# Optimization experiments

Measured on AMD Instinct MI355X. Metric: run time of the kernel, lower is better.

## Reference

```python
import jax, jax.numpy as jnp
import numpy as np

B, S, D = 4, 2048, 2048
H = 16
HD = D // H  # head_dim = 128


def setup_inputs() -> dict:
    key = jax.random.key(0)
    ks = jax.random.split(key, 6)
    x = jax.random.normal(ks[0], (B, S, D), dtype=jnp.float32)
    Wq = jax.random.normal(ks[1], (D, D), dtype=jnp.float32) * 0.02
    Wk = jax.random.normal(ks[2], (D, D), dtype=jnp.float32) * 0.02
    Wv = jax.random.normal(ks[3], (D, D), dtype=jnp.float32) * 0.02
    Wo = jax.random.normal(ks[4], (D, D), dtype=jnp.float32) * 0.02
    bo = jax.random.normal(ks[5], (D,), dtype=jnp.float32) * 0.02
    return {"x": x, "Wq": Wq, "Wk": Wk, "Wv": Wv, "Wo": Wo, "bo": bo}


def reference(x, Wq, Wk, Wv, Wo, bo):
    b, s, _ = x.shape
    # QKV projections, split heads: [b, h, s, hd]
    q = (x @ Wq).reshape(b, s, H, HD).transpose(0, 2, 1, 3)
    k = (x @ Wk).reshape(b, s, H, HD).transpose(0, 2, 1, 3)
    v = (x @ Wv).reshape(b, s, H, HD).transpose(0, 2, 1, 3)
    # scores: [b, h, s_q, s_k]
    scores = jnp.einsum("bhqd,bhkd->bhqk", q, k)
    # causal mask: future positions (k > q) get -inf (masking before scaling,
    # as in the original; -inf is invariant under the scale)
    causal = jnp.tril(jnp.ones((s, s), dtype=bool))
    scores = jnp.where(causal, scores, -jnp.inf)
    scale = 1.0 / np.sqrt(HD).astype(np.float32)
    attn = jax.nn.softmax(scores * scale, axis=-1)
    # dropout p=0.0 -> identity (eval-mode reference)
    ctx = jnp.einsum("bhqk,bhkd->bqhd", attn, v).reshape(b, s, D)
    return ctx @ Wo + bo
```

## Files before the change

### kernel.cpp

```cpp
#include <hip/hip_runtime.h>
#include <hip/hip_bf16.h>

#define BB 4
#define SS 2048
#define DD 2048
#define HH 16
#define HDD 128

typedef __bf16 bf16x8_t __attribute__((ext_vector_type(8)));
typedef float f32x4 __attribute__((ext_vector_type(4)));
typedef float f32x16 __attribute__((ext_vector_type(16)));

static __device__ __forceinline__ unsigned short f2bf(float f) {
    union { float f; unsigned u; } v; v.f = f;
    unsigned r = v.u + 0x7fffu + ((v.u >> 16) & 1u);
    return (unsigned short)(r >> 16);
}

static __device__ __forceinline__ unsigned cvtpk_bf16(float lo, float hiv) {
    unsigned r;
    asm("v_cvt_pk_bf16_f32 %0, %1, %2" : "=v"(r) : "v"(lo), "v"(hiv));
    return r;
}

static __device__ __forceinline__ void pl32swap(unsigned& a, unsigned& b) {
    auto rr = __builtin_amdgcn_permlane32_swap((int)a, (int)b, false, false);
    a = (unsigned)rr[0];
    b = (unsigned)rr[1];
}

static __device__ __forceinline__ void gload_lds16(const void* g, void* lds) {
    __builtin_amdgcn_global_load_lds(
        (const __attribute__((address_space(1))) void*)g,
        (__attribute__((address_space(3))) void*)lds, 16, 0, 0);
}

__global__ void convert_x(const float* __restrict__ x, unsigned short* __restrict__ xb, int n) {
    int i = (blockIdx.x * blockDim.x + threadIdx.x) * 4;
    int stride = gridDim.x * blockDim.x * 4;
    for (; i < n; i += stride) {
        float4 v = *(const float4*)(x + i);
        ushort4 o;
        o.x = f2bf(v.x); o.y = f2bf(v.y); o.z = f2bf(v.z); o.w = f2bf(v.w);
        *(ushort4*)(xb + i) = o;
    }
}

__global__ void transpose_w(const float* __restrict__ Wq, const float* __restrict__ Wk,
                            const float* __restrict__ Wv, const float* __restrict__ Wo,
                            unsigned short* __restrict__ WqkvT, unsigned short* __restrict__ WoT) {
    __shared__ float t[32][33];
    const int z = blockIdx.z;
    const float* W = (z == 0) ? Wq : (z == 1) ? Wk : (z == 2) ? Wv : Wo;
    unsigned short* T = (z < 3) ? (WqkvT + (size_t)z * DD * DD) : WoT;
    const int k0 = blockIdx.x * 32, n0 = blockIdx.y * 32;
    const int tx = threadIdx.x, ty = threadIdx.y;
#pragma unroll
    for (int i = 0; i < 4; ++i) {
        int r = ty + i * 8;
        t[r][tx] = W[(size_t)(k0 + r) * DD + n0 + tx];
    }
    __syncthreads();
#pragma unroll
    for (int i = 0; i < 4; ++i) {
        int r = ty + i * 8;
        T[(size_t)(n0 + r) * DD + k0 + tx] = f2bf(t[tx][r]);
    }
}

template <int MODE>
__global__ __launch_bounds__(512, 1) void gemm256(
    const unsigned short* __restrict__ A, const unsigned short* __restrict__ BT,
    unsigned short* __restrict__ outQ, unsigned short* __restrict__ outK,
    unsigned short* __restrict__ outV, float* __restrict__ outF,
    const float* __restrict__ bias) {
    __shared__ __attribute__((aligned(16))) char lds[131072];
    const int tid = threadIdx.x, l = tid & 63;
    const int w = tid >> 6;
    const int wr = w >> 2, wc = w & 3;
    const int nwg = gridDim.x * gridDim.y;
    int lin = blockIdx.y * gridDim.x + blockIdx.x;
    lin = (lin & 7) * (nwg >> 3) + (lin >> 3);
    const int m0 = (lin / gridDim.x) * 256;
    const int n0 = (lin % gridDim.x) * 256;

    f32x4 acc[8][4] = {};

    const int rowl = tid >> 3, c16s = tid & 7;
    const int sw16 = (c16s ^ (rowl & 7)) * 16;
    const char* aSrc[4];
    const char* bSrc[4];
#pragma unroll
    for (int rg = 0; rg < 4; ++rg) {
        aSrc[rg] = (const char*)A + ((size_t)(m0 + rg * 64 + rowl) * 2048) * 2 + sw16;
        bSrc[rg] = (const char*)BT + ((size_t)(n0 + rg * 64 + rowl) * 2048) * 2 + sw16;
    }
    const int dstOff = tid * 16;

    auto stage = [&](int slot, int off) {
        char* sA = lds + slot * 32768;
        char* sB = lds + 65536 + slot * 32768;
        gload_lds16(bSrc[0] + off, sB + 0 * 8192 + dstOff);
        gload_lds16(bSrc[1] + off, sB + 1 * 8192 + dstOff);
        gload_lds16(bSrc[2] + off, sB + 2 * 8192 + dstOff);
        gload_lds16(bSrc[3] + off, sB + 3 * 8192 + dstOff);
        gload_lds16(aSrc[0] + off, sA + 0 * 8192 + dstOff);
        gload_lds16(aSrc[2] + off, sA + 2 * 8192 + dstOff);
        gload_lds16(aSrc[1] + off, sA + 1 * 8192 + dstOff);
        gload_lds16(aSrc[3] + off, sA + 3 * 8192 + dstOff);
    };

    stage(0, 0);
    asm volatile("s_waitcnt vmcnt(0)" ::: "memory");
    __builtin_amdgcn_s_barrier();

    const int lr = l & 15, hi4 = l >> 4;
    int cur = 0;
    for (int t = 0; t < 32; ++t) {
        const char* As_ = lds + cur * 32768;
        const char* Bs_ = lds + 65536 + cur * 32768;
        bf16x8_t aa[4], bb[4];
#pragma unroll
        for (int mq = 0; mq < 4; ++mq) {
            int row = wr * 128 + mq * 16 + lr;
            aa[mq] = *(const bf16x8_t*)(As_ + row * 128 + ((hi4) ^ (row & 7)) * 16);
        }
#pragma unroll
        for (int nq = 0; nq < 4; ++nq) {
            int col = wc * 64 + nq * 16 + lr;
            bb[nq] = *(const bf16x8_t*)(Bs_ + col * 128 + ((hi4) ^ (col & 7)) * 16);
        }
        if (t + 1 < 32) stage(cur ^ 1, (t + 1) * 128);
        __builtin_amdgcn_s_setprio(1);
#pragma unroll
        for (int mq = 0; mq < 4; ++mq)
#pragma unroll
            for (int nq = 0; nq < 4; ++nq)
                acc[mq][nq] = __builtin_amdgcn_mfma_f32_16x16x32_bf16(aa[mq], bb[nq], acc[mq][nq], 0, 0, 0);
        __builtin_amdgcn_s_setprio(0);
        if (t + 1 < 32) { asm volatile("s_waitcnt vmcnt(8)" ::: "memory"); }
        else            { asm volatile("s_waitcnt vmcnt(0)" ::: "memory"); }
        __builtin_amdgcn_s_barrier();
#pragma unroll
        for (int mq = 0; mq < 4; ++mq) {
            int row = wr * 128 + 64 + mq * 16 + lr;
            aa[mq] = *(const bf16x8_t*)(As_ + row * 128 + ((hi4) ^ (row & 7)) * 16);
        }
        __builtin_amdgcn_s_setprio(1);
#pragma unroll
        for (int mq = 0; mq < 4; ++mq)
#pragma unroll
            for (int nq = 0; nq < 4; ++nq)
                acc[4 + mq][nq] = __builtin_amdgcn_mfma_f32_16x16x32_bf16(aa[mq], bb[nq], acc[4 + mq][nq], 0, 0, 0);
        __builtin_amdgcn_s_setprio(0);
#pragma unroll
        for (int nq = 0; nq < 4; ++nq) {
            int col = wc * 64 + nq * 16 + lr;
            bb[nq] = *(const bf16x8_t*)(Bs_ + col * 128 + ((4 + hi4) ^ (col & 7)) * 16);
        }
#pragma unroll
        for (int mq = 0; mq < 4; ++mq) {
            int row = wr * 128 + mq * 16 + lr;
            aa[mq] = *(const bf16x8_t*)(As_ + row * 128 + ((4 + hi4) ^ (row & 7)) * 16);
        }
        __builtin_amdgcn_s_setprio(1);
#pragma unroll
        for (int mq = 0; mq < 4; ++mq)
#pragma unroll
            for (int nq = 0; nq < 4; ++nq)
                acc[mq][nq] = __builtin_amdgcn_mfma_f32_16x16x32_bf16(aa[mq], bb[nq], acc[mq][nq], 0, 0, 0);
        __builtin_amdgcn_s_setprio(0);
#pragma unroll
        for (int mq = 0; mq < 4; ++mq) {
            int row = wr * 128 + 64 + mq * 16 + lr;
            aa[mq] = *(const bf16x8_t*)(As_ + row * 128 + ((4 + hi4) ^ (row & 7)) * 16);
        }
        __builtin_amdgcn_s_setprio(1);
#pragma unroll
        for (int mq = 0; mq < 4; ++mq)
#pragma unroll
            for (int nq = 0; nq < 4; ++nq)
                acc[4 + mq][nq] = __builtin_amdgcn_mfma_f32_16x16x32_bf16(aa[mq], bb[nq], acc[4 + mq][nq], 0, 0, 0);
        __builtin_amdgcn_s_setprio(0);
        if (t + 1 < 32) { asm volatile("s_waitcnt vmcnt(2)" ::: "memory"); }
        __builtin_amdgcn_s_barrier();
        cur ^= 1;
    }

    const int rbase = m0 + wr * 128 + (hi4 << 2);
    const int cbase = n0 + wc * 64 + lr;
    if (MODE == 0) {
#pragma unroll
        for (int nq = 0; nq < 4; ++nq) {
            int col = cbase + nq * 16;
            int mat = col >> 11;
            int nn = col & 2047;
            int h = nn >> 7, hd = nn & 127;
            if (mat == 2) {
#pragma unroll
                for (int i = 0; i < 8; ++i) {
                    int row = rbase + i * 16;
                    int b = row >> 11, s = row & 2047;
                    ushort4 pk;
                    pk.x = f2bf(acc[i][nq][0]); pk.y = f2bf(acc[i][nq][1]);
                    pk.z = f2bf(acc[i][nq][2]); pk.w = f2bf(acc[i][nq][3]);
                    *(ushort4*)(outV + ((size_t)(b * HH + h) * HDD + hd) * SS + s) = pk;
                }
            } else {
                unsigned short* outp = mat ? outK : outQ;
#pragma unroll
                for (int i = 0; i < 8; ++i) {
#pragma unroll
                    for (int r = 0; r < 4; ++r) {
                        int row = rbase + i * 16 + r;
                        int b = row >> 11, s = row & 2047;
                        outp[((size_t)(b * HH + h) * SS + s) * HDD + hd] = f2bf(acc[i][nq][r]);
                    }
                }
            }
        }
    } else {
#pragma unroll
        for (int nq = 0; nq < 4; ++nq) {
            int col = cbase + nq * 16;
            float bv = bias[col];
#pragma unroll
            for (int i = 0; i < 8; ++i) {
#pragma unroll
                for (int r = 0; r < 4; ++r) {
                    int row = rbase + i * 16 + r;
                    outF[(size_t)row * DD + col] = acc[i][nq][r] + bv;
                }
            }
        }
    }
}

__global__ __launch_bounds__(256, 2) void attn_kernel(
    const unsigned short* __restrict__ Q, const unsigned short* __restrict__ K,
    const unsigned short* __restrict__ VT, unsigned short* __restrict__ ctx) {
    __shared__ __attribute__((aligned(16))) unsigned short Ks[2][64 * 128];
    __shared__ __attribute__((aligned(16))) unsigned short Vs[2][128 * 64];
    __shared__ float Al[4][32];
    const int tid = threadIdx.x, w = tid >> 6, l = tid & 63;
    const int hi = l >> 5, l31 = l & 31;
    const int hb = hi * 16;
    const int swz = (l31 & 7) << 4;
    const int p = blockIdx.x, h = blockIdx.y, b = blockIdx.z;
    const int bh = b * HH + h;
    const float scale2 = 0.08838834764831845f * 1.4426950408889634f;

    const unsigned short* Qbh = Q + (size_t)bh * SS * HDD;
    const char* Kbh = (const char*)(K + (size_t)bh * SS * HDD);
    const char* Vbh = (const char*)(VT + (size_t)bh * HDD * SS);

    const char* kbase[4];
    const char* vbase[4];
#pragma unroll
    for (int i = 0; i < 4; ++i) {
        int cp = (i * 256 + tid) * 16;
        int krow = cp >> 8, kcb = cp & 255;
        kbase[i] = Kbh + (size_t)krow * 256 + (kcb ^ ((krow & 7) << 4));
        int vrow = cp >> 7, vcb = cp & 127;
        vbase[i] = Vbh + (size_t)vrow * (SS * 2) + (vcb ^ ((vrow & 7) << 4));
    }

    auto stage = [&](int buf, int kv0) {
#pragma unroll
        for (int i = 0; i < 4; ++i) {
            int cp = (i * 256 + tid) * 16;
            gload_lds16(kbase[i] + (size_t)kv0 * 256, (char*)&Ks[buf][0] + cp);
            gload_lds16(vbase[i] + (size_t)kv0 * 2, (char*)&Vs[buf][0] + cp);
        }
    };

    for (int pass = 0; pass < 2; ++pass) {
        const int qt = pass ? p : 15 - p;
        const int q0w = qt * 128 + w * 32;
        const int qabs = q0w + l31;
        const int nkv = 2 * qt + 2;

        bf16x8_t qf[8];
#pragma unroll
        for (int ds = 0; ds < 8; ++ds)
            qf[ds] = *(const bf16x8_t*)(Qbh + (size_t)qabs * HDD + ds * 16 + hi * 8);

        float m_r = -1e30f, l_r = 0.f;
        f32x16 o0 = {}, o1 = {}, o2 = {}, o3 = {};

        int buf = 0;
        stage(0, 0);
        __syncthreads();

        for (int kt = 0; kt < nkv; ++kt) {
            const int kv0 = kt * 64;
            if (kt + 1 < nkv) stage(buf ^ 1, kv0 + 64);

            if (kv0 <= q0w + 31) {
                const char* Kb = (const char*)&Ks[buf][0];
                const char* Vb = (const char*)&Vs[buf][0];
                f32x16 s0 = {}, s1 = {};
                {
                    bf16x8_t kf[8];
                    const int rb = l31 * 256;
#pragma unroll
                    for (int ds = 0; ds < 8; ++ds)
                        kf[ds] = *(const bf16x8_t*)(Kb + rb + ((ds * 32 + hb) ^ swz));
                    __builtin_amdgcn_s_setprio(1);
#pragma unroll
                    for (int ds = 0; ds < 8; ++ds)
                        s0 = __builtin_amdgcn_mfma_f32_32x32x16_bf16(kf[ds], qf[ds], s0, 0, 0, 0);
                    __builtin_amdgcn_s_setprio(0);
#pragma unroll
                    for (int ds = 0; ds < 8; ++ds)
                        kf[ds] = *(const bf16x8_t*)(Kb + rb + 32 * 256 + ((ds * 32 + hb) ^ swz));
                    __builtin_amdgcn_s_setprio(1);
#pragma unroll
                    for (int ds = 0; ds < 8; ++ds)
                        s1 = __builtin_amdgcn_mfma_f32_32x32x16_bf16(kf[ds], qf[ds], s1, 0, 0, 0);
                    __builtin_amdgcn_s_setprio(0);
                }

                if (kv0 + 63 > q0w) {
                    const int qrel = qabs - kv0;
#pragma unroll
                    for (int r = 0; r < 16; ++r) {
                        const int kl = (r & 3) + 8 * (r >> 2) + 4 * hi;
                        s0[r] = (kl > qrel) ? -1e30f : s0[r] * scale2;
                        s1[r] = (kl + 32 > qrel) ? -1e30f : s1[r] * scale2;
                    }
                } else {
#pragma unroll
                    for (int r = 0; r < 16; ++r) { s0[r] *= scale2; s1[r] *= scale2; }
                }

                float mx = s0[0];
#pragma unroll
                for (int r = 1; r < 16; ++r) mx = fmaxf(mx, s0[r]);
#pragma unroll
                for (int r = 0; r < 16; ++r) mx = fmaxf(mx, s1[r]);
                {
                    unsigned mu = __float_as_uint(mx), mu2 = mu;
                    pl32swap(mu, mu2);
                    mx = fmaxf(__uint_as_float(mu), __uint_as_float(mu2));
                }

                if (__any(mx - m_r > 8.f)) {
                    float mnew = fmaxf(m_r, mx);
                    float alpha = exp2f(m_r - mnew);
                    m_r = mnew;
                    l_r *= alpha;
                    Al[w][l31] = alpha;
#pragma unroll
                    for (int r = 0; r < 16; ++r) {
                        float ar = Al[w][(r & 3) + 8 * (r >> 2) + 4 * hi];
                        o0[r] *= ar; o1[r] *= ar; o2[r] *= ar; o3[r] *= ar;
                    }
                }

                float ps = 0.f;
#pragma unroll
                for (int r = 0; r < 16; ++r) { s0[r] = exp2f(s0[r] - m_r); ps += s0[r]; }
#pragma unroll
                for (int r = 0; r < 16; ++r) { s1[r] = exp2f(s1[r] - m_r); ps += s1[r]; }
                {
                    unsigned pu = __float_as_uint(ps), pu2 = pu;
                    pl32swap(pu, pu2);
                    l_r += __uint_as_float(pu) + __uint_as_float(pu2);
                }

                bf16x8_t pa[4];
                {
                    union { unsigned u[4]; bf16x8_t v; } uu;
#define MK_PA(SV, BASE, OUT)                                     \
                    {                                            \
                        unsigned X0 = cvtpk_bf16(SV[BASE + 0], SV[BASE + 1]); \
                        unsigned Y0 = cvtpk_bf16(SV[BASE + 4], SV[BASE + 5]); \
                        pl32swap(X0, Y0);                        \
                        unsigned X1 = cvtpk_bf16(SV[BASE + 2], SV[BASE + 3]); \
                        unsigned Y1 = cvtpk_bf16(SV[BASE + 6], SV[BASE + 7]); \
                        pl32swap(X1, Y1);                        \
                        uu.u[0] = X0; uu.u[1] = X1; uu.u[2] = Y0; uu.u[3] = Y1; \
                        OUT = uu.v;                              \
                    }
                    MK_PA(s0, 0, pa[0]);
                    MK_PA(s0, 8, pa[1]);
                    MK_PA(s1, 0, pa[2]);
                    MK_PA(s1, 8, pa[3]);
#undef MK_PA
                }

#pragma unroll
                for (int ks = 0; ks < 4; ++ks) {
                    bf16x8_t vf[4];
#pragma unroll
                    for (int dsub = 0; dsub < 4; ++dsub)
                        vf[dsub] = *(const bf16x8_t*)(Vb + (dsub * 32 + l31) * 128 + ((ks * 32 + hb) ^ swz));
                    __builtin_amdgcn_s_setprio(1);
                    o0 = __builtin_amdgcn_mfma_f32_32x32x16_bf16(pa[ks], vf[0], o0, 0, 0, 0);
                    o1 = __builtin_amdgcn_mfma_f32_32x32x16_bf16(pa[ks], vf[1], o1, 0, 0, 0);
                    o2 = __builtin_amdgcn_mfma_f32_32x32x16_bf16(pa[ks], vf[2], o2, 0, 0, 0);
                    o3 = __builtin_amdgcn_mfma_f32_32x32x16_bf16(pa[ks], vf[3], o3, 0, 0, 0);
                    __builtin_amdgcn_s_setprio(0);
                }
            }
            __syncthreads();
            buf ^= 1;
        }

        Al[w][l31] = 1.f / l_r;
        unsigned short* cb_ = ctx + (size_t)b * SS * DD + (size_t)h * HDD;
#pragma unroll
        for (int r = 0; r < 16; ++r) {
            const int ql = (r & 3) + 8 * (r >> 2) + 4 * hi;
            float inv = Al[w][ql];
            const size_t rowoff = (size_t)(q0w + ql) * DD;
            cb_[rowoff + 0 * 32 + l31] = f2bf(o0[r] * inv);
            cb_[rowoff + 1 * 32 + l31] = f2bf(o1[r] * inv);
            cb_[rowoff + 2 * 32 + l31] = f2bf(o2[r] * inv);
            cb_[rowoff + 3 * 32 + l31] = f2bf(o3[r] * inv);
        }
    }
}

extern "C" void kernel_launch(void* const* d_in, const int* in_sizes, int n_in,
                              void* d_out, int out_size, void* d_ws, size_t ws_size,
                              hipStream_t stream) {
    (void)in_sizes; (void)n_in; (void)out_size; (void)ws_size;
    const float* x  = (const float*)d_in[0];
    const float* Wq = (const float*)d_in[1];
    const float* Wk = (const float*)d_in[2];
    const float* Wv = (const float*)d_in[3];
    const float* Wo = (const float*)d_in[4];
    const float* bo = (const float*)d_in[5];

    char* ws = (char*)d_ws;
    unsigned short* xb    = (unsigned short*)(ws);
    unsigned short* WqkvT = (unsigned short*)(ws + (32u << 20));
    unsigned short* WoT   = (unsigned short*)(ws + (56u << 20));
    unsigned short* Qb    = (unsigned short*)(ws + (64u << 20));
    unsigned short* Kb    = (unsigned short*)(ws + (96u << 20));
    unsigned short* VTb   = (unsigned short*)(ws + (160u << 20));
    unsigned short* ctx   = xb;

    convert_x<<<4096, 256, 0, stream>>>(x, xb, BB * SS * DD);
    transpose_w<<<dim3(64, 64, 4), dim3(32, 8), 0, stream>>>(Wq, Wk, Wv, Wo, WqkvT, WoT);
    gemm256<0><<<dim3(24, 32), 512, 0, stream>>>(xb, WqkvT, Qb, Kb, VTb, nullptr, nullptr);
    attn_kernel<<<dim3(8, HH, BB), 256, 0, stream>>>(Qb, Kb, VTb, ctx);
    gemm256<1><<<dim3(8, 32), 512, 0, stream>>>(ctx, WoT, nullptr, nullptr, nullptr, (float*)d_out, bo);
}
```

Before: 426.2 us.

## Split GEMM K-tiles into half-tiles and interleave loads with MFMA phases

Restructures the 256x256 GEMM main loop so each K=64 tile is stored as two 32-wide half-tiles with a 4-way swizzle. Global-to-LDS loads for future half-tiles are issued between the four MFMA phases, so prefetch runs up to two tiles ahead instead of one. The goal is finer-grained overlap of memory traffic with MFMA work and shorter waits at the loop boundary. In exchange it adds more barriers and lgkmcnt waits per iteration. The loop tail also reissues loads for clamped tile indices, which is redundant work.

```diff
diff --git a/kernel.cpp b/kernel.cpp
--- a/kernel.cpp
+++ b/kernel.cpp
@@ -86,107 +86,123 @@
 
     f32x4 acc[8][4] = {};
 
-    const int rowl = tid >> 3, c16s = tid & 7;
-    const int sw16 = (c16s ^ (rowl & 7)) * 16;
-    const char* aSrc[4];
-    const char* bSrc[4];
-#pragma unroll
-    for (int rg = 0; rg < 4; ++rg) {
-        aSrc[rg] = (const char*)A + ((size_t)(m0 + rg * 64 + rowl) * 2048) * 2 + sw16;
-        bSrc[rg] = (const char*)BT + ((size_t)(n0 + rg * 64 + rowl) * 2048) * 2 + sw16;
-    }
-    const int dstOff = tid * 16;
-
-    auto stage = [&](int slot, int off) {
-        char* sA = lds + slot * 32768;
-        char* sB = lds + 65536 + slot * 32768;
-        gload_lds16(bSrc[0] + off, sB + 0 * 8192 + dstOff);
-        gload_lds16(bSrc[1] + off, sB + 1 * 8192 + dstOff);
-        gload_lds16(bSrc[2] + off, sB + 2 * 8192 + dstOff);
-        gload_lds16(bSrc[3] + off, sB + 3 * 8192 + dstOff);
-        gload_lds16(aSrc[0] + off, sA + 0 * 8192 + dstOff);
-        gload_lds16(aSrc[2] + off, sA + 2 * 8192 + dstOff);
-        gload_lds16(aSrc[1] + off, sA + 1 * 8192 + dstOff);
-        gload_lds16(aSrc[3] + off, sA + 3 * 8192 + dstOff);
+    const int srow = tid >> 2;
+    const int swz16 = ((tid & 3) ^ (srow & 3)) << 4;
+    const char* aR = (const char*)A + ((size_t)(m0 + srow) * 2048) * 2 + swz16;
+    const char* bR = (const char*)BT + ((size_t)(n0 + srow) * 2048) * 2 + swz16;
+    const int dOff = tid * 16;
+
+    auto stA = [&](int slot, int kt, int kh) {
+        char* d = lds + slot * 32768 + kh * 16384 + dOff;
+        const char* s = aR + kt * 128 + kh * 64;
+        gload_lds16(s, d);
+        gload_lds16(s + (size_t)128 * 4096, d + 8192);
     };
-
-    stage(0, 0);
-    asm volatile("s_waitcnt vmcnt(0)" ::: "memory");
+    auto stB = [&](int slot, int kt, int kh) {
+        char* d = lds + 65536 + slot * 32768 + kh * 16384 + dOff;
+        const char* s = bR + kt * 128 + kh * 64;
+        gload_lds16(s, d);
+        gload_lds16(s + (size_t)128 * 4096, d + 8192);
+    };
+
+    stA(0, 0, 0); stB(0, 0, 0); stA(0, 0, 1); stB(0, 0, 1); stA(1, 1, 0); stB(1, 1, 0);
+    asm volatile("s_waitcnt vmcnt(8)" ::: "memory");
     __builtin_amdgcn_s_barrier();
 
-    const int lr = l & 15, hi4 = l >> 4;
-    int cur = 0;
+    const int lr = l & 15;
+    const int rsw = (((l >> 4) ^ (lr & 3)) << 4);
+
     for (int t = 0; t < 32; ++t) {
-        const char* As_ = lds + cur * 32768;
-        const char* Bs_ = lds + 65536 + cur * 32768;
+        const int slot = t & 1;
+        const char* As_ = lds + slot * 32768;
+        const char* Bs_ = lds + 65536 + slot * 32768;
+        const int tn1 = (t + 1 < 32) ? t + 1 : 31;
+        const int tn2 = (t + 2 < 32) ? t + 2 : 31;
+        const int sl1 = (t + 1) & 1;
         bf16x8_t aa[4], bb[4];
-#pragma unroll
-        for (int mq = 0; mq < 4; ++mq) {
-            int row = wr * 128 + mq * 16 + lr;
-            aa[mq] = *(const bf16x8_t*)(As_ + row * 128 + ((hi4) ^ (row & 7)) * 16);
+
+#pragma unroll
+        for (int ii = 0; ii < 4; ++ii) {
+            int row = wr * 128 + ii * 16 + lr;
+            aa[ii] = *(const bf16x8_t*)(As_ + row * 64 + rsw);
         }
 #pragma unroll
         for (int nq = 0; nq < 4; ++nq) {
             int col = wc * 64 + nq * 16 + lr;
-            bb[nq] = *(const bf16x8_t*)(Bs_ + col * 128 + ((hi4) ^ (col & 7)) * 16);
-        }
-        if (t + 1 < 32) stage(cur ^ 1, (t + 1) * 128);
+            bb[nq] = *(const bf16x8_t*)(Bs_ + col * 64 + rsw);
+        }
+        stA(sl1, tn1, 1);
+        __builtin_amdgcn_s_barrier();
+        asm volatile("s_waitcnt lgkmcnt(0)");
         __builtin_amdgcn_s_setprio(1);
 #pragma unroll
-        for (int mq = 0; mq < 4; ++mq)
+        for (int ii = 0; ii < 4; ++ii)
 #pragma unroll
             for (int nq = 0; nq < 4; ++nq)
-                acc[mq][nq] = __builtin_amdgcn_mfma_f32_16x16x32_bf16(aa[mq], bb[nq], acc[mq][nq], 0, 0, 0);
+                acc[ii][nq] = __builtin_amdgcn_mfma_f32_16x16x32_bf16(aa[ii], bb[nq], acc[ii][nq], 0, 0, 0);
         __builtin_amdgcn_s_setprio(0);
-        if (t + 1 < 32) { asm volatile("s_waitcnt vmcnt(8)" ::: "memory"); }
-        else            { asm volatile("s_waitcnt vmcnt(0)" ::: "memory"); }
-        __builtin_amdgcn_s_barrier();
-#pragma unroll
-        for (int mq = 0; mq < 4; ++mq) {
-            int row = wr * 128 + 64 + mq * 16 + lr;
-            aa[mq] = *(const bf16x8_t*)(As_ + row * 128 + ((hi4) ^ (row & 7)) * 16);
-        }
+        __builtin_amdgcn_s_barrier();
+
+#pragma unroll
+        for (int ii = 0; ii < 4; ++ii) {
+            int row = wr * 128 + 64 + ii * 16 + lr;
+            aa[ii] = *(const bf16x8_t*)(As_ + row * 64 + rsw);
+        }
+        stB(sl1, tn1, 1);
+        __builtin_amdgcn_s_barrier();
+        asm volatile("s_waitcnt lgkmcnt(0)");
         __builtin_amdgcn_s_setprio(1);
 #pragma unroll
-        for (int mq = 0; mq < 4; ++mq)
+        for (int ii = 0; ii < 4; ++ii)
 #pragma unroll
             for (int nq = 0; nq < 4; ++nq)
-                acc[4 + mq][nq] = __builtin_amdgcn_mfma_f32_16x16x32_bf16(aa[mq], bb[nq], acc[4 + mq][nq], 0, 0, 0);
+                acc[4 + ii][nq] = __builtin_amdgcn_mfma_f32_16x16x32_bf16(aa[ii], bb[nq], acc[4 + ii][nq], 0, 0, 0);
         __builtin_amdgcn_s_setprio(0);
+        asm volatile("s_waitcnt vmcnt(8)" ::: "memory");
+        __builtin_amdgcn_s_barrier();
+
+#pragma unroll
+        for (int ii = 0; ii < 4; ++ii) {
+            int row = wr * 128 + ii * 16 + lr;
+            aa[ii] = *(const bf16x8_t*)(As_ + 16384 + row * 64 + rsw);
+        }
 #pragma unroll
         for (int nq = 0; nq < 4; ++nq) {
             int col = wc * 64 + nq * 16 + lr;
-            bb[nq] = *(const bf16x8_t*)(Bs_ + col * 128 + ((4 + hi4) ^ (col & 7)) * 16);
-        }
-#pragma unroll
-        for (int mq = 0; mq < 4; ++mq) {
-            int row = wr * 128 + mq * 16 + lr;
-            aa[mq] = *(const bf16x8_t*)(As_ + row * 128 + ((4 + hi4) ^ (row & 7)) * 16);
-        }
+            bb[nq] = *(const bf16x8_t*)(Bs_ + 16384 + col * 64 + rsw);
+        }
+        stA(slot, tn2, 0);
+        __builtin_amdgcn_s_barrier();
+        asm volatile("s_waitcnt lgkmcnt(0)");
         __builtin_amdgcn_s_setprio(1);
 #pragma unroll
-        for (int mq = 0; mq < 4; ++mq)
+        for (int ii = 0; ii < 4; ++ii)
 #pragma unroll
             for (int nq = 0; nq < 4; ++nq)
-                acc[mq][nq] = __builtin_amdgcn_mfma_f32_16x16x32_bf16(aa[mq], bb[nq], acc[mq][nq], 0, 0, 0);
+                acc[ii][nq] = __builtin_amdgcn_mfma_f32_16x16x32_bf16(aa[ii], bb[nq], acc[ii][nq], 0, 0, 0);
         __builtin_amdgcn_s_setprio(0);
-#pragma unroll
-        for (int mq = 0; mq < 4; ++mq) {
-            int row = wr * 128 + 64 + mq * 16 + lr;
-            aa[mq] = *(const bf16x8_t*)(As_ + row * 128 + ((4 + hi4) ^ (row & 7)) * 16);
-        }
+        __builtin_amdgcn_s_barrier();
+
+#pragma unroll
+        for (int ii = 0; ii < 4; ++ii) {
+            int row = wr * 128 + 64 + ii * 16 + lr;
+            aa[ii] = *(const bf16x8_t*)(As_ + 16384 + row * 64 + rsw);
+        }
+        stB(slot, tn2, 0);
+        __builtin_amdgcn_s_barrier();
+        asm volatile("s_waitcnt lgkmcnt(0)");
         __builtin_amdgcn_s_setprio(1);
 #pragma unroll
-        for (int mq = 0; mq < 4; ++mq)
+        for (int ii = 0; ii < 4; ++ii)
 #pragma unroll
             for (int nq = 0; nq < 4; ++nq)
-                acc[4 + mq][nq] = __builtin_amdgcn_mfma_f32_16x16x32_bf16(aa[mq], bb[nq], acc[4 + mq][nq], 0, 0, 0);
+                acc[4 + ii][nq] = __builtin_amdgcn_mfma_f32_16x16x32_bf16(aa[ii], bb[nq], acc[4 + ii][nq], 0, 0, 0);
         __builtin_amdgcn_s_setprio(0);
-        if (t + 1 < 32) { asm volatile("s_waitcnt vmcnt(2)" ::: "memory"); }
-        __builtin_amdgcn_s_barrier();
-        cur ^= 1;
-    }
-
+        asm volatile("s_waitcnt vmcnt(8)" ::: "memory");
+        __builtin_amdgcn_s_barrier();
+    }
+
+    const int hi4 = l >> 4;
     const int rbase = m0 + wr * 128 + (hi4 << 2);
     const int cbase = n0 + wc * 64 + lr;
     if (MODE == 0) {
```

New measurement: 449.9 us. 1.06x slower.
